# Optimization experiments

Measured on AMD Instinct MI355X. Metric: run time of the kernel, lower is better.

The kernel has to match this reference:

```python
import jax, jax.numpy as jnp
import numpy as np

T, B, D = 512, 32, 1024


def setup_inputs() -> dict:
    key = jax.random.key(0)
    kx, kwh, kwx, kwg = jax.random.split(key, 4)
    x = jax.random.normal(kx, (T, B, D), dtype=jnp.float32)
    # W_h: orthogonal init scaled by 0.5
    a = jax.random.normal(kwh, (D, D), dtype=jnp.float32)
    q, r = jnp.linalg.qr(a)
    W_h = 0.5 * q * jnp.sign(jnp.diag(r))[None, :]
    # xavier uniform for W_x, W_g: bound = sqrt(6/(D+D))
    bound = float(np.sqrt(6.0 / (D + D)))
    W_x = jax.random.uniform(kwx, (D, D), minval=-bound, maxval=bound, dtype=jnp.float32)
    W_g = jax.random.uniform(kwg, (D, D), minval=-bound, maxval=bound, dtype=jnp.float32)
    b = jnp.zeros((D,), dtype=jnp.float32)
    b_g = jnp.zeros((D,), dtype=jnp.float32)
    return {"x": x, "W_h": W_h, "W_x": W_x, "W_g": W_g, "b": b, "b_g": b_g}


def reference(x, W_h, W_x, W_g, b, b_g):
    # x: [T, B, D]
    Tn, Bn, Dn = x.shape
    # Precompute input projections (batched over T*B, like the torch code)
    Wx_all = jnp.einsum('tbd,ed->tbe', x, W_x)                      # [T,B,D]
    gate_all = jax.nn.sigmoid(jnp.einsum('tbd,ed->tbe', x, W_g) + b_g)  # [T,B,D]
    h0 = jnp.zeros((Bn, Dn), dtype=x.dtype)

    def step(h_prev, inp):
        wx_t, g_t = inp
        pre_act = h_prev @ W_h.T + wx_t + b
        h_new = h_prev + g_t * jnp.tanh(pre_act)
        out_t = h_new * jax.nn.silu(h_new)
        return h_new, (h_new, out_t)

    _, (h_seq, output) = jax.lax.scan(step, h0, (Wx_all, gate_all))
    h = jnp.concatenate([h0[None], h_seq], axis=0)  # [T+1,B,D]
    return output, h
```

## Files before the change

### kernel.cpp

```cpp
#include <hip/hip_runtime.h>
#include <hip/hip_bf16.h>
#include <stdint.h>


#define T_DIM 512
#define B_DIM 32
#define D_DIM 1024
#define M_DIM (T_DIM*B_DIM)

typedef __attribute__((ext_vector_type(4))) float f32x4;
typedef __attribute__((ext_vector_type(8))) short bf16x8;

__device__ inline unsigned short f2b(float f){
  union { float f; uint32_t u; } c; c.f = f;
  uint32_t u = c.u + 0x7fffu + ((c.u >> 16) & 1u);
  return (unsigned short)(u >> 16);
}
__device__ inline float b2f(unsigned short h){
  union { uint32_t u; float f; } c; c.u = ((uint32_t)h) << 16;
  return c.f;
}

__global__ void init_kernel(float* __restrict__ out_h0,
                            float* __restrict__ h_ex,
                            uint32_t* __restrict__ flags){
  int i = blockIdx.x*blockDim.x + threadIdx.x;
  out_h0[i] = 0.f;
  int g = i >> 12, j = i & 4095;
  h_ex[(size_t)g*8192 + j] = 0.f;
  if (i < 4096) flags[i] = 0;
}

template<int MODE>
__global__ __launch_bounds__(256, 2)
void proj_m(const float* __restrict__ X, const float* __restrict__ W,
            const float* __restrict__ bias, float* __restrict__ OUT)
{
  __shared__ unsigned short Ah[128*64];
  __shared__ unsigned short Al[128*64];
  __shared__ unsigned short Bh[128*64];
  __shared__ unsigned short Bl[128*64];
  char* AhB=(char*)Ah; char* AlB=(char*)Al; char* BhB=(char*)Bh; char* BlB=(char*)Bl;
  const int tid  = threadIdx.x;
  const int lane = tid & 63;
  const int wave = tid >> 6;
  const int m0 = blockIdx.y * 128;
  const int n0 = blockIdx.x * 128;
  const int wm = (wave >> 1) * 64;
  const int wn = (wave & 1) * 64;
  const int fr = lane & 15;
  const int fq = lane >> 4;

  f32x4 acc[4][4];
  #pragma unroll
  for (int i=0;i<4;++i)
    #pragma unroll
    for (int j=0;j<4;++j) acc[i][j] = (f32x4){0.f,0.f,0.f,0.f};

  for (int kt = 0; kt < D_DIM/64; ++kt) {
    #pragma unroll
    for (int c = 0; c < 4; ++c) {
      int idx = tid + c*256;
      int row = idx >> 3;
      int k8  = idx & 7;
      const float* ga = X + (size_t)(m0+row)*D_DIM + kt*64 + k8*8;
      const float* gb = W + (size_t)(n0+row)*D_DIM + kt*64 + k8*8;
      f32x4 a0 = *(const f32x4*)ga, a1 = *(const f32x4*)(ga+4);
      f32x4 b0 = *(const f32x4*)gb, b1 = *(const f32x4*)(gb+4);
      bf16x8 vah, val, vbh, vbl;
      #pragma unroll
      for (int j=0;j<4;++j){
        unsigned short h;
        h = f2b(a0[j]); vah[j]   = (short)h; val[j]   = (short)f2b(a0[j]-b2f(h));
        h = f2b(a1[j]); vah[4+j] = (short)h; val[4+j] = (short)f2b(a1[j]-b2f(h));
        h = f2b(b0[j]); vbh[j]   = (short)h; vbl[j]   = (short)f2b(b0[j]-b2f(h));
        h = f2b(b1[j]); vbh[4+j] = (short)h; vbl[4+j] = (short)f2b(b1[j]-b2f(h));
      }
      int lb = row*128 + ((k8*16) ^ ((row&7)<<4));
      *(bf16x8*)(AhB + lb) = vah;
      *(bf16x8*)(AlB + lb) = val;
      *(bf16x8*)(BhB + lb) = vbh;
      *(bf16x8*)(BlB + lb) = vbl;
    }
    __syncthreads();
    #pragma unroll
    for (int kk=0; kk<2; ++kk) {
      bf16x8 afh[4], afl[4], bfh[4], bfl[4];
      #pragma unroll
      for (int i=0;i<4;++i){
        int row = wm+i*16+fr;
        int off = row*128 + ((kk*64 + fq*16) ^ ((row&7)<<4));
        afh[i] = *(const bf16x8*)(AhB + off);
        afl[i] = *(const bf16x8*)(AlB + off);
      }
      #pragma unroll
      for (int j=0;j<4;++j){
        int row = wn+j*16+fr;
        int off = row*128 + ((kk*64 + fq*16) ^ ((row&7)<<4));
        bfh[j] = *(const bf16x8*)(BhB + off);
        bfl[j] = *(const bf16x8*)(BlB + off);
      }
      #pragma unroll
      for (int i=0;i<4;++i)
        #pragma unroll
        for (int j=0;j<4;++j){
          acc[i][j] = __builtin_amdgcn_mfma_f32_16x16x32_bf16(afh[i], bfh[j], acc[i][j], 0,0,0);
          acc[i][j] = __builtin_amdgcn_mfma_f32_16x16x32_bf16(afh[i], bfl[j], acc[i][j], 0,0,0);
          acc[i][j] = __builtin_amdgcn_mfma_f32_16x16x32_bf16(afl[i], bfh[j], acc[i][j], 0,0,0);
        }
    }
    __syncthreads();
  }
  #pragma unroll
  for (int j=0;j<4;++j) {
    int col = n0 + wn + j*16 + fr;
    float bv = bias[col];
    #pragma unroll
    for (int i=0;i<4;++i) {
      int rowb = m0 + wm + i*16 + fq*4;
      #pragma unroll
      for (int r=0;r<4;++r) {
        float v = acc[i][j][r] + bv;
        if (MODE==1) v = 1.f/(1.f + expf(-v));
        OUT[(size_t)(rowb+r)*D_DIM + col] = v;
      }
    }
  }
}

__global__ __launch_bounds__(256, 1)
void rnn_persist(const float* __restrict__ Wh,
                 float* PO,
                 float* PH,
                 float* __restrict__ h_ex,
                 uint32_t* __restrict__ flags)
{
  __shared__ char  hsb[4*4096];
  __shared__ float part[16*137];

  const int tid = threadIdx.x;
  const int blk = blockIdx.x;
  const int g   = blk & 7;
  const int sl  = blk >> 3;
  const int e0  = sl * 32;
  const int b0  = g * 4;
  const int e2  = tid & 15;
  const int kc  = tid >> 4;

  f32x4 wh0[16], wh1[16];
  {
    const f32x4* wp0 = (const f32x4*)(Wh + (size_t)(e0 + 2*e2 + 0)*D_DIM + kc*64);
    const f32x4* wp1 = (const f32x4*)(Wh + (size_t)(e0 + 2*e2 + 1)*D_DIM + kc*64);
    #pragma unroll
    for (int i = 0; i < 16; ++i) { wh0[i] = wp0[i]; wh1[i] = wp1[i]; }
  }

  const int bl = tid >> 5;
  const int el = tid & 31;
  float hold = 0.f;

  for (int t = 0; t < T_DIM; ++t) {
    size_t idx_out = (size_t)t*32768 + (size_t)(b0 + bl)*D_DIM + e0 + el;
    float Pv = 0.f, Gv = 0.f;
    if (tid < 128) {
      Pv = PH[idx_out + 32768];
      Gv = PO[idx_out];
    }

    if (t > 0 && tid < 32) {
      const uint32_t* fp = flags + (size_t)(g*32 + tid)*16;
      uint32_t v;
      while (true) {
        asm volatile("global_load_dword %0, %1, off sc1" : "=v"(v) : "v"(fp) : "memory");
        asm volatile("s_waitcnt vmcnt(0)" ::: "memory");
        if (v >= (uint32_t)t) break;
        __builtin_amdgcn_s_sleep(1);
      }
    }
    __syncthreads();

    {
      const char* hsrc = (const char*)(h_ex + (size_t)(g*2 + (t&1))*4096) + tid*16;
      f32x4 r0, r1, r2, r3;
      asm volatile("global_load_dwordx4 %0, %1, off sc1" : "=v"(r0) : "v"(hsrc)         : "memory");
      asm volatile("global_load_dwordx4 %0, %1, off sc1" : "=v"(r1) : "v"(hsrc + 4096)  : "memory");
      asm volatile("global_load_dwordx4 %0, %1, off sc1" : "=v"(r2) : "v"(hsrc + 8192)  : "memory");
      asm volatile("global_load_dwordx4 %0, %1, off sc1" : "=v"(r3) : "v"(hsrc + 12288) : "memory");
      asm volatile("s_waitcnt vmcnt(0)" ::: "memory");
      __builtin_amdgcn_sched_barrier(0);
      #pragma unroll
      for (int i = 0; i < 4; ++i) {
        int G   = i*256 + tid;
        int bq  = G >> 8;
        int g16 = G & 255;
        int g16s = g16 ^ (g16 >> 4);
        f32x4 v = (i==0) ? r0 : (i==1) ? r1 : (i==2) ? r2 : r3;
        *(f32x4*)(hsb + bq*4096 + g16s*16) = v;
      }
    }
    __syncthreads();

    float acc[4][2];
    #pragma unroll
    for (int b = 0; b < 4; ++b) { acc[b][0] = 0.f; acc[b][1] = 0.f; }
    #pragma unroll
    for (int i = 0; i < 16; ++i) {
      f32x4 w0 = wh0[i], w1 = wh1[i];
      #pragma unroll
      for (int b = 0; b < 4; ++b) {
        f32x4 hv = *(const f32x4*)(hsb + b*4096 + kc*256 + ((i ^ kc) << 4));
        float d0 = hv[0]*w0[0] + hv[1]*w0[1] + hv[2]*w0[2] + hv[3]*w0[3];
        float d1 = hv[0]*w1[0] + hv[1]*w1[1] + hv[2]*w1[2] + hv[3]*w1[3];
        acc[b][0] += d0;
        acc[b][1] += d1;
      }
    }
    #pragma unroll
    for (int b = 0; b < 4; ++b) {
      part[kc*137 + b*32 + 2*e2 + 0] = acc[b][0];
      part[kc*137 + b*32 + 2*e2 + 1] = acc[b][1];
    }
    __syncthreads();

    float hn = 0.f, sg = 0.f;
    if (tid < 128) {
      float pre = 0.f;
      #pragma unroll
      for (int q = 0; q < 16; ++q) pre += part[q*137 + bl*32 + el];
      pre += Pv;
      float th = tanhf(pre);
      hn = hold + Gv*th;
      hold = hn;
      sg = 1.f/(1.f + expf(-hn));
      float* hdst = h_ex + (size_t)(g*2 + ((t+1)&1))*4096 + bl*1024 + e0 + el;
      asm volatile("global_store_dword %0, %1, off sc1" :: "v"(hdst), "v"(hn) : "memory");
    }
    asm volatile("s_waitcnt vmcnt(0)" ::: "memory");
    __syncthreads();

    if (tid == 0) {
      uint32_t fv = (uint32_t)(t+1);
      uint32_t* fptr = flags + (size_t)(g*32 + sl)*16;
      asm volatile("global_store_dword %0, %1, off sc1" :: "v"(fptr), "v"(fv) : "memory");
    }

    if (tid < 128) {
      PO[idx_out] = hn*hn*sg;
      PH[idx_out + 32768] = hn;
    }
  }
}

extern "C" void kernel_launch(void* const* d_in, const int* in_sizes, int n_in,
                              void* d_out, int out_size, void* d_ws, size_t ws_size,
                              hipStream_t stream) {
  const float* x  = (const float*)d_in[0];
  const float* Wh = (const float*)d_in[1];
  const float* Wx = (const float*)d_in[2];
  const float* Wg = (const float*)d_in[3];
  const float* b  = (const float*)d_in[4];
  const float* bg = (const float*)d_in[5];

  float* out_o = (float*)d_out;
  float* out_h = out_o + (size_t)M_DIM*D_DIM;

  char* ws = (char*)d_ws;
  float*    h_ex  = (float*)ws;
  uint32_t* flags = (uint32_t*)(ws + (256<<10));

  init_kernel<<<128, 256, 0, stream>>>(out_h, h_ex, flags);
  proj_m<1><<<dim3(8,128), 256, 0, stream>>>(x, Wg, bg, out_o);
  proj_m<0><<<dim3(8,128), 256, 0, stream>>>(x, Wx, b,  out_h + 32768);
  rnn_persist<<<256, 256, 0, stream>>>(Wh, out_o, out_h, h_ex, flags);
}
```

Before: 1.912 ms.

## Prefetch next-step inputs and offload output writes to idle warps

Loads the precomputed projection and gate values for the next timestep right after the flag store, so they are in flight across the barrier instead of being loaded at the top of each step. Moves the flag polling to warp 2, and hands the silu output and hidden-state stores to warp 3 via a small shared buffer with paired float2 writes. Warps 0-1 stay on the serial critical path. The added shared-memory staging introduces a possible hazard: warp 3 reads hout after the barrier while warps 0-1 may already be rewriting it in the next step. That ordering is covered only by the later barriers.

```diff
diff --git a/kernel.cpp b/kernel.cpp
--- a/kernel.cpp
+++ b/kernel.cpp
@@ -9,6 +9,7 @@
 #define M_DIM (T_DIM*B_DIM)
 
 typedef __attribute__((ext_vector_type(4))) float f32x4;
+typedef __attribute__((ext_vector_type(2))) float f32x2;
 typedef __attribute__((ext_vector_type(8))) short bf16x8;
 
 __device__ inline unsigned short f2b(float f){
@@ -137,6 +138,7 @@
 {
   __shared__ char  hsb[4*4096];
   __shared__ float part[16*137];
+  __shared__ float hout[128];
 
   const int tid = threadIdx.x;
   const int blk = blockIdx.x;
@@ -159,16 +161,18 @@
   const int el = tid & 31;
   float hold = 0.f;
 
+  float Pv = 0.f, Gv = 0.f;
+  if (tid < 128) {
+    size_t idx0 = (size_t)(b0 + bl)*D_DIM + e0 + el;
+    Pv = PH[idx0 + 32768];
+    Gv = PO[idx0];
+  }
+
   for (int t = 0; t < T_DIM; ++t) {
     size_t idx_out = (size_t)t*32768 + (size_t)(b0 + bl)*D_DIM + e0 + el;
-    float Pv = 0.f, Gv = 0.f;
-    if (tid < 128) {
-      Pv = PH[idx_out + 32768];
-      Gv = PO[idx_out];
-    }
-
-    if (t > 0 && tid < 32) {
-      const uint32_t* fp = flags + (size_t)(g*32 + tid)*16;
+
+    if (t > 0 && tid >= 128 && tid < 160) {
+      const uint32_t* fp = flags + (size_t)(g*32 + (tid - 128))*16;
       uint32_t v;
       while (true) {
         asm volatile("global_load_dword %0, %1, off sc1" : "=v"(v) : "v"(fp) : "memory");
@@ -222,16 +226,15 @@
     }
     __syncthreads();
 
-    float hn = 0.f, sg = 0.f;
     if (tid < 128) {
       float pre = 0.f;
       #pragma unroll
       for (int q = 0; q < 16; ++q) pre += part[q*137 + bl*32 + el];
       pre += Pv;
       float th = tanhf(pre);
-      hn = hold + Gv*th;
+      float hn = hold + Gv*th;
       hold = hn;
-      sg = 1.f/(1.f + expf(-hn));
+      hout[tid] = hn;
       float* hdst = h_ex + (size_t)(g*2 + ((t+1)&1))*4096 + bl*1024 + e0 + el;
       asm volatile("global_store_dword %0, %1, off sc1" :: "v"(hdst), "v"(hn) : "memory");
     }
@@ -244,9 +247,25 @@
       asm volatile("global_store_dword %0, %1, off sc1" :: "v"(fptr), "v"(fv) : "memory");
     }
 
-    if (tid < 128) {
-      PO[idx_out] = hn*hn*sg;
-      PH[idx_out + 32768] = hn;
+    if (t + 1 < T_DIM && tid < 128) {
+      size_t idx_n = (size_t)(t+1)*32768 + (size_t)(b0 + bl)*D_DIM + e0 + el;
+      Pv = PH[idx_n + 32768];
+      Gv = PO[idx_n];
+    }
+
+    if (tid >= 192) {
+      int j  = tid - 192;
+      int bb = j >> 4;
+      int ep = (j & 15) * 2;
+      float h0v = hout[bb*32 + ep];
+      float h1v = hout[bb*32 + ep + 1];
+      f32x2 ov, hv2;
+      ov[0] = h0v*h0v*(1.f/(1.f + expf(-h0v)));
+      ov[1] = h1v*h1v*(1.f/(1.f + expf(-h1v)));
+      hv2[0] = h0v; hv2[1] = h1v;
+      size_t ixw = (size_t)t*32768 + (size_t)(b0 + bb)*D_DIM + e0 + ep;
+      *(f32x2*)(PO + ixw) = ov;
+      *(f32x2*)(PH + ixw + 32768) = hv2;
     }
   }
 }
```

After: 2.107 ms. 10.2% more time.
